# Performance work log

Hardware: AMD Instinct MI355X
Metric: run time of the kernel (lower is better)

Reference implementation:

```python
import jax, jax.numpy as jnp
import numpy as np

EPS = 1e-5
N_NODES = 50000


def sage_conv(x, src, dst, Wl, Wr, b):
    # mean-aggregate source features at destination nodes, then two linears
    msgs = x[src]  # [E, F] irregular gather
    agg = jax.ops.segment_sum(msgs, dst, num_segments=N_NODES)
    cnt = jax.ops.segment_sum(jnp.ones((src.shape[0], 1), x.dtype), dst,
                              num_segments=N_NODES)
    agg = agg / jnp.maximum(cnt, 1.0)
    return agg @ Wl + x @ Wr + b


def batch_norm(h, gamma, beta):
    mu = jnp.mean(h, axis=0)
    var = jnp.mean((h - mu) ** 2, axis=0)  # biased var, as torch BN training
    return (h - mu) * jax.lax.rsqrt(var + EPS) * gamma + beta


def setup_inputs() -> dict:
    key = jax.random.key(0)
    ks = jax.random.split(key, 16)
    d_in, d_h, n_cls, n_edges = 128, 128, 2, 600000
    s = lambda fan: 1.0 / np.sqrt(fan)
    inp = {
        "x": jax.random.normal(ks[0], (N_NODES, d_in), jnp.float32),
        "edge_index": jax.random.randint(ks[1], (2, n_edges), 0, N_NODES, jnp.int64),
        "W_l0": jax.random.uniform(ks[2], (d_in, d_h), jnp.float32, -s(d_in), s(d_in)),
        "W_r0": jax.random.uniform(ks[3], (d_in, d_h), jnp.float32, -s(d_in), s(d_in)),
        "b0": jnp.zeros((d_h,), jnp.float32),
        "g0": jnp.ones((d_h,), jnp.float32),
        "be0": jnp.zeros((d_h,), jnp.float32),
        "W_l1": jax.random.uniform(ks[4], (d_h, d_h), jnp.float32, -s(d_h), s(d_h)),
        "W_r1": jax.random.uniform(ks[5], (d_h, d_h), jnp.float32, -s(d_h), s(d_h)),
        "b1": jnp.zeros((d_h,), jnp.float32),
        "g1": jnp.ones((d_h,), jnp.float32),
        "be1": jnp.zeros((d_h,), jnp.float32),
        "W_out": jax.random.uniform(ks[6], (d_h, n_cls), jnp.float32, -s(d_h), s(d_h)),
        "b_out": jnp.zeros((n_cls,), jnp.float32),
    }
    return inp


def reference(x, edge_index, W_l0, W_r0, b0, g0, be0,
              W_l1, W_r1, b1, g1, be1, W_out, b_out):
    src, dst = edge_index[0], edge_index[1]
    # layer 0: SAGEConv -> BN -> ReLU (dropout = identity in eval/reference)
    h = sage_conv(x, src, dst, W_l0, W_r0, b0)
    h = jax.nn.relu(batch_norm(h, g0, be0))
    # layer 1
    h = sage_conv(h, src, dst, W_l1, W_r1, b1)
    h = jax.nn.relu(batch_norm(h, g1, be1))
    return h @ W_out + b_out
```

## Files before the change

kernel.cpp:

```cpp
#include <hip/hip_runtime.h>
#include <hip/hip_bf16.h>

#define F 128

typedef __attribute__((ext_vector_type(8))) short short8;
typedef __attribute__((ext_vector_type(4))) float floatx4;

__device__ __forceinline__ float bf_lo(unsigned u) { return __uint_as_float(u << 16); }
__device__ __forceinline__ float bf_hi(unsigned u) { return __uint_as_float(u & 0xffff0000u); }

__device__ __forceinline__ unsigned short f2bf(float x) {
  unsigned u = __float_as_uint(x);
  u += 0x7fffu + ((u >> 16) & 1u);
  return (unsigned short)(u >> 16);
}
__device__ __forceinline__ unsigned pack2(float a, float b) {
  return (unsigned)f2bf(a) | ((unsigned)f2bf(b) << 16);
}
__device__ __forceinline__ void add8(float* a, uint4 u) {
  a[0] += bf_lo(u.x); a[1] += bf_hi(u.x);
  a[2] += bf_lo(u.y); a[3] += bf_hi(u.y);
  a[4] += bf_lo(u.z); a[5] += bf_hi(u.z);
  a[6] += bf_lo(u.w); a[7] += bf_hi(u.w);
}

__global__ __launch_bounds__(256) void k_pre(const int* __restrict__ dst, int* __restrict__ A,
                                             int E, int cb,
                                             const float* __restrict__ x,
                                             const float* __restrict__ Wl0,
                                             const float* __restrict__ Wr0,
                                             const float* __restrict__ Wl1,
                                             const float* __restrict__ Wr1,
                                             unsigned short* __restrict__ xb,
                                             unsigned short* __restrict__ WcatT0,
                                             unsigned short* __restrict__ WcatT1, int n4) {
  if (blockIdx.x < cb) {
    int e = blockIdx.x * 256 + threadIdx.x;
    if (e < E) atomicAdd(&A[dst[e]], 1);
    return;
  }
  int i = (blockIdx.x - cb) * 256 + threadIdx.x;
  if (i < n4) {
    float4 v = ((const float4*)x)[i];
    ((ushort4*)xb)[i] = make_ushort4(f2bf(v.x), f2bf(v.y), f2bf(v.z), f2bf(v.w));
  } else {
    int j = i - n4;
    if (j < 2 * 256 * F) {
      int layer = j >> 15;
      int jj = j & 32767;
      int k = jj >> 7, n = jj & (F - 1);
      const float* Wl = layer ? Wl1 : Wl0;
      const float* Wr = layer ? Wr1 : Wr0;
      unsigned short* WT = layer ? WcatT1 : WcatT0;
      float v = (k < F) ? Wl[k * F + n] : Wr[(k - F) * F + n];
      WT[(size_t)n * 256 + k] = f2bf(v);
    }
  }
}

__global__ __launch_bounds__(1024) void k_scan(int* __restrict__ A, int* __restrict__ bsum,
                                               int* __restrict__ bases, int* __restrict__ ctl,
                                               int n, int nb) {
  __shared__ int wtot[16];
  __shared__ int lastS, sbase;
  int t = threadIdx.x, l = t & 63, w = t >> 6;
  int i = blockIdx.x * 1024 + t;
  int v = (i < n) ? A[i] : 0;
  int acc = v;
#pragma unroll
  for (int off = 1; off < 64; off <<= 1) {
    int u = __shfl_up(acc, off);
    if (l >= off) acc += u;
  }
  if (l == 63) wtot[w] = acc;
  __syncthreads();
  int woff = 0, total = 0;
#pragma unroll
  for (int ww = 0; ww < 16; ++ww) {
    total += wtot[ww];
    if (ww < w) woff += wtot[ww];
  }
  int local = woff + (acc - v);
  if (t == 0) {
    __hip_atomic_store(&bsum[blockIdx.x], total, __ATOMIC_RELEASE, __HIP_MEMORY_SCOPE_AGENT);
    int tk = __hip_atomic_fetch_add(&ctl[0], 1, __ATOMIC_ACQ_REL, __HIP_MEMORY_SCOPE_AGENT);
    lastS = (tk == nb - 1);
  }
  __syncthreads();
  if (lastS) {
    if (t < 64) {
      int bv = (t < nb) ? __hip_atomic_load(&bsum[t], __ATOMIC_ACQUIRE, __HIP_MEMORY_SCOPE_AGENT) : 0;
      int a2 = bv;
#pragma unroll
      for (int off = 1; off < 64; off <<= 1) {
        int u = __shfl_up(a2, off);
        if (t >= off) a2 += u;
      }
      if (t < nb)
        __hip_atomic_store(&bases[t], a2 - bv, __ATOMIC_RELAXED, __HIP_MEMORY_SCOPE_AGENT);
    }
    __syncthreads();
    if (t == 0) {
      __threadfence();
      __hip_atomic_store(&ctl[1], 1, __ATOMIC_RELEASE, __HIP_MEMORY_SCOPE_AGENT);
    }
  }
  if (t == 0) {
    while (__hip_atomic_load(&ctl[1], __ATOMIC_ACQUIRE, __HIP_MEMORY_SCOPE_AGENT) == 0) {}
    sbase = __hip_atomic_load(&bases[blockIdx.x], __ATOMIC_RELAXED, __HIP_MEMORY_SCOPE_AGENT);
  }
  __syncthreads();
  if (i < n) A[i] = local + sbase;
}

__global__ __launch_bounds__(256) void k_fill(const int* __restrict__ srcT,
                                              const int* __restrict__ dst,
                                              int* __restrict__ A, int* __restrict__ adj, int E) {
  int e = blockIdx.x * 256 + threadIdx.x;
  if (e >= E) return;
  int s = srcT[e], d = dst[e];
  int slot = atomicAdd(&A[d], 1);
  adj[slot] = s;
}

__global__ __launch_bounds__(256) void k_gather(const unsigned short* __restrict__ xin,
                                                const int* __restrict__ A,
                                                const int* __restrict__ adj,
                                                unsigned short* __restrict__ aggb, int N) {
  int base = blockIdx.x * 8 + ((threadIdx.x >> 6) << 1);
  int l = threadIdx.x & 63;
  int grp = l >> 4, ln = l & 15;
  const uint4* xrows = (const uint4*)xin;

  int d0 = base, d1 = base + 1;
  bool v0 = d0 < N, v1 = d1 < N;
  int e00 = 0, e01 = 0, e10 = 0, e11 = 0;
  if (v0) { e00 = (d0 == 0) ? 0 : A[d0 - 1]; e01 = A[d0]; }
  if (v1) { e10 = A[d1 - 1]; e11 = A[d1]; }
  int deg0 = e01 - e00, deg1 = e11 - e10;
  int ids0 = 0, ids1 = 0;
  if (v0 && deg0 > 0) ids0 = adj[min(e00 + l, e01 - 1)];
  if (v1 && deg1 > 0) ids1 = adj[min(e10 + l, e11 - 1)];
  int m0 = (v0 && deg0 > 0) ? min(deg0, 64) : 0;
  int m1 = (v1 && deg1 > 0) ? min(deg1, 64) : 0;
  int mm = max(m0, m1);

  float acc0[8] = {0.f, 0.f, 0.f, 0.f, 0.f, 0.f, 0.f, 0.f};
  float acc1[8] = {0.f, 0.f, 0.f, 0.f, 0.f, 0.f, 0.f, 0.f};
  for (int j0 = 0; j0 < mm; j0 += 4) {
    int jj = j0 + grp;
    int s0 = __shfl(ids0, jj);
    int s1 = __shfl(ids1, jj);
    if (jj < m0) { uint4 u = xrows[(size_t)s0 * 16 + ln]; add8(acc0, u); }
    if (jj < m1) { uint4 u = xrows[(size_t)s1 * 16 + ln]; add8(acc1, u); }
  }
  for (int e = e00 + 64 + grp; e < e01; e += 4) {
    int s = adj[e];
    uint4 u = xrows[(size_t)s * 16 + ln];
    add8(acc0, u);
  }
  for (int e = e10 + 64 + grp; e < e11; e += 4) {
    int s = adj[e];
    uint4 u = xrows[(size_t)s * 16 + ln];
    add8(acc1, u);
  }
#pragma unroll
  for (int k2 = 0; k2 < 8; ++k2) {
    acc0[k2] += __shfl_xor(acc0[k2], 16);
    acc0[k2] += __shfl_xor(acc0[k2], 32);
    acc1[k2] += __shfl_xor(acc1[k2], 16);
    acc1[k2] += __shfl_xor(acc1[k2], 32);
  }
  if (grp == 0) {
    if (v0) {
      float inv = 1.0f / fmaxf((float)deg0, 1.0f);
      uint4 o = make_uint4(pack2(acc0[0] * inv, acc0[1] * inv), pack2(acc0[2] * inv, acc0[3] * inv),
                           pack2(acc0[4] * inv, acc0[5] * inv), pack2(acc0[6] * inv, acc0[7] * inv));
      ((uint4*)aggb)[(size_t)d0 * 16 + ln] = o;
    }
    if (v1) {
      float inv = 1.0f / fmaxf((float)deg1, 1.0f);
      uint4 o = make_uint4(pack2(acc1[0] * inv, acc1[1] * inv), pack2(acc1[2] * inv, acc1[3] * inv),
                           pack2(acc1[4] * inv, acc1[5] * inv), pack2(acc1[6] * inv, acc1[7] * inv));
      ((uint4*)aggb)[(size_t)d1 * 16 + ln] = o;
    }
  }
}

__global__ __launch_bounds__(256, 2) void k_gemm(
    const unsigned short* __restrict__ aggb, const unsigned short* __restrict__ xb,
    const unsigned short* __restrict__ WcatT, const float* __restrict__ bias,
    unsigned short* __restrict__ hb, float* __restrict__ pbuf, int N) {
  const int w = threadIdx.x >> 6;
  const int l = threadIdx.x & 63;
  const int lm = l & 15;
  const int lq = l >> 4;
  const int cbase = 32 * w;

  short8 bfrag[2][8];
#pragma unroll
  for (int c = 0; c < 2; ++c) {
    int col = cbase + 16 * c + lm;
    const unsigned short* wp = WcatT + (size_t)col * 256 + lq * 8;
#pragma unroll
    for (int s = 0; s < 8; ++s) bfrag[c][s] = *(const short8*)(wp + 32 * s);
  }
  float bcol0 = bias[cbase + lm];
  float bcol1 = bias[cbase + 16 + lm];
  float bsum0 = 0.f, bsum1 = 0.f, bsq0 = 0.f, bsq1 = 0.f;

  int r0 = blockIdx.x * 64;
  floatx4 acc[4][2] = {};
#pragma unroll
  for (int t = 0; t < 4; ++t) {
    int r = r0 + 16 * t + lm;
    const unsigned short* arow = aggb + (size_t)r * F + lq * 8;
    const unsigned short* xrow = xb + (size_t)r * F + lq * 8;
    short8 af[8];
#pragma unroll
    for (int s = 0; s < 4; ++s) {
      af[s] = *(const short8*)(arow + 32 * s);
      af[s + 4] = *(const short8*)(xrow + 32 * s);
    }
#pragma unroll
    for (int s = 0; s < 8; ++s) {
      acc[t][0] = __builtin_amdgcn_mfma_f32_16x16x32_bf16(af[s], bfrag[0][s], acc[t][0], 0, 0, 0);
      acc[t][1] = __builtin_amdgcn_mfma_f32_16x16x32_bf16(af[s], bfrag[1][s], acc[t][1], 0, 0, 0);
    }
  }
#pragma unroll
  for (int t = 0; t < 4; ++t) {
#pragma unroll
    for (int c = 0; c < 2; ++c) {
      int col = cbase + 16 * c + lm;
      float bc = c ? bcol1 : bcol0;
#pragma unroll
      for (int g = 0; g < 4; ++g) {
        int row = r0 + 16 * t + lq * 4 + g;
        if (row < N) {
          float v = acc[t][c][g] + bc;
          hb[(size_t)row * F + col] = f2bf(v);
          if (c) { bsum1 += v; bsq1 += v * v; }
          else   { bsum0 += v; bsq0 += v * v; }
        }
      }
    }
  }
  bsum0 += __shfl_xor(bsum0, 16); bsum0 += __shfl_xor(bsum0, 32);
  bsq0  += __shfl_xor(bsq0, 16);  bsq0  += __shfl_xor(bsq0, 32);
  bsum1 += __shfl_xor(bsum1, 16); bsum1 += __shfl_xor(bsum1, 32);
  bsq1  += __shfl_xor(bsq1, 16);  bsq1  += __shfl_xor(bsq1, 32);
  if (lq == 0) {
    float* pb = pbuf + (size_t)blockIdx.x * 256;
    pb[cbase + lm]            = bsum0;
    pb[128 + cbase + lm]      = bsq0;
    pb[cbase + 16 + lm]       = bsum1;
    pb[128 + cbase + 16 + lm] = bsq1;
  }
}

__global__ __launch_bounds__(256) void k_bnstats(const float* __restrict__ pbuf,
                                                 const float* __restrict__ g,
                                                 const float* __restrict__ be,
                                                 float* __restrict__ stats,
                                                 float* __restrict__ scale,
                                                 float* __restrict__ shift,
                                                 float invN, int nb) {
  int t = threadIdx.x;
  float s = 0.f;
  for (int b = blockIdx.x; b < nb; b += 8) s += pbuf[(size_t)b * 256 + t];
  atomicAdd(&stats[t], s);
  __threadfence();
  __syncthreads();
  __shared__ int lastS;
  if (t == 0) {
    int ticket = atomicAdd((int*)(stats + 256), 1);
    lastS = (ticket == 7);
  }
  __syncthreads();
  if (lastS) {
    __threadfence();
    if (t < 128) {
      float sum = __hip_atomic_load(&stats[t], __ATOMIC_RELAXED, __HIP_MEMORY_SCOPE_AGENT);
      float sq  = __hip_atomic_load(&stats[t + 128], __ATOMIC_RELAXED, __HIP_MEMORY_SCOPE_AGENT);
      float mu = sum * invN;
      float var = fmaxf(sq * invN - mu * mu, 0.0f);
      float sc = g[t] * rsqrtf(var + 1e-5f);
      scale[t] = sc;
      shift[t] = be[t] - mu * sc;
    }
  }
}

__global__ __launch_bounds__(256) void k_bnrelu(const unsigned short* __restrict__ h,
                                                unsigned short* __restrict__ dst,
                                                const float* __restrict__ scale,
                                                const float* __restrict__ shift, int n8) {
  int i = blockIdx.x * 256 + threadIdx.x;
  if (i >= n8) return;
  uint4 u = ((const uint4*)h)[i];
  int g = i & 15;
  float4 sc0 = ((const float4*)scale)[2 * g];
  float4 sc1 = ((const float4*)scale)[2 * g + 1];
  float4 sh0 = ((const float4*)shift)[2 * g];
  float4 sh1 = ((const float4*)shift)[2 * g + 1];
  unsigned o0 = pack2(fmaxf(fmaf(bf_lo(u.x), sc0.x, sh0.x), 0.f),
                      fmaxf(fmaf(bf_hi(u.x), sc0.y, sh0.y), 0.f));
  unsigned o1 = pack2(fmaxf(fmaf(bf_lo(u.y), sc0.z, sh0.z), 0.f),
                      fmaxf(fmaf(bf_hi(u.y), sc0.w, sh0.w), 0.f));
  unsigned o2 = pack2(fmaxf(fmaf(bf_lo(u.z), sc1.x, sh1.x), 0.f),
                      fmaxf(fmaf(bf_hi(u.z), sc1.y, sh1.y), 0.f));
  unsigned o3 = pack2(fmaxf(fmaf(bf_lo(u.w), sc1.z, sh1.z), 0.f),
                      fmaxf(fmaf(bf_hi(u.w), sc1.w, sh1.w), 0.f));
  ((uint4*)dst)[i] = make_uint4(o0, o1, o2, o3);
}

__global__ __launch_bounds__(256) void k_bnout(const unsigned short* __restrict__ hb,
                                               const float* __restrict__ scale,
                                               const float* __restrict__ shift,
                                               const float* __restrict__ Wout,
                                               const float* __restrict__ bout,
                                               float* __restrict__ out, int N) {
  __shared__ float W0s[F], W1s[F];
  int t = threadIdx.x;
  if (t < F) {
    W0s[t] = Wout[2 * t];
    W1s[t] = Wout[2 * t + 1];
  }
  __syncthreads();
  int r = blockIdx.x * 16 + (t >> 4);
  int ln = t & 15;
  if (r >= N) return;
  uint4 u = ((const uint4*)(hb + (size_t)r * F))[ln];
  float4 sc0 = ((const float4*)scale)[2 * ln];
  float4 sc1 = ((const float4*)scale)[2 * ln + 1];
  float4 sh0 = ((const float4*)shift)[2 * ln];
  float4 sh1 = ((const float4*)shift)[2 * ln + 1];
  float v[8];
  v[0] = fmaxf(fmaf(bf_lo(u.x), sc0.x, sh0.x), 0.f);
  v[1] = fmaxf(fmaf(bf_hi(u.x), sc0.y, sh0.y), 0.f);
  v[2] = fmaxf(fmaf(bf_lo(u.y), sc0.z, sh0.z), 0.f);
  v[3] = fmaxf(fmaf(bf_hi(u.y), sc0.w, sh0.w), 0.f);
  v[4] = fmaxf(fmaf(bf_lo(u.z), sc1.x, sh1.x), 0.f);
  v[5] = fmaxf(fmaf(bf_hi(u.z), sc1.y, sh1.y), 0.f);
  v[6] = fmaxf(fmaf(bf_lo(u.w), sc1.z, sh1.z), 0.f);
  v[7] = fmaxf(fmaf(bf_hi(u.w), sc1.w, sh1.w), 0.f);
  float a0 = 0.f, a1 = 0.f;
#pragma unroll
  for (int j = 0; j < 8; ++j) {
    a0 += v[j] * W0s[8 * ln + j];
    a1 += v[j] * W1s[8 * ln + j];
  }
#pragma unroll
  for (int off = 1; off < 16; off <<= 1) {
    a0 += __shfl_xor(a0, off);
    a1 += __shfl_xor(a1, off);
  }
  if (ln == 0) {
    out[2 * r]     = a0 + bout[0];
    out[2 * r + 1] = a1 + bout[1];
  }
}

extern "C" void kernel_launch(void* const* d_in, const int* in_sizes, int n_in,
                              void* d_out, int out_size, void* d_ws, size_t ws_size,
                              hipStream_t stream) {
  const float* x   = (const float*)d_in[0];
  const int*   eix = (const int*)d_in[1];
  const float* Wl0 = (const float*)d_in[2];
  const float* Wr0 = (const float*)d_in[3];
  const float* b0  = (const float*)d_in[4];
  const float* g0  = (const float*)d_in[5];
  const float* be0 = (const float*)d_in[6];
  const float* Wl1 = (const float*)d_in[7];
  const float* Wr1 = (const float*)d_in[8];
  const float* b1  = (const float*)d_in[9];
  const float* g1  = (const float*)d_in[10];
  const float* be1 = (const float*)d_in[11];
  const float* Wo  = (const float*)d_in[12];
  const float* bo  = (const float*)d_in[13];

  int N = in_sizes[0] / F;
  int E = in_sizes[1] / 2;
  const int* src  = eix;
  const int* dstv = eix + E;

  int nRowBlocks = (N + 63) / 64;
  size_t Npad = (size_t)nRowBlocks * 64;
  int nScanB = (N + 1023) / 1024;

  unsigned short* aggb   = (unsigned short*)d_ws;
  unsigned short* xb     = aggb + Npad * F;
  unsigned short* hb     = xb + Npad * F;
  unsigned short* WcatT0 = hb + Npad * F;
  unsigned short* WcatT1 = WcatT0 + 256 * F;
  float* scale  = (float*)(WcatT1 + 256 * F);
  float* shift  = scale + F;
  int*   A      = (int*)(shift + F);
  int*   bsum   = A + N;
  int*   bases  = bsum + 64;
  int*   ctl    = bases + 64;
  float* stats0 = (float*)(ctl + 4);
  float* stats1 = stats0 + 257;
  int*   adj    = (int*)(stats1 + 257);
  float* pbuf   = (float*)(adj + E);

  hipMemsetAsync(A, 0, (size_t)(N + 132 + 514) * sizeof(int), stream);

  int n4 = N * F / 4, n8 = N * F / 8;
  int cb = (E + 255) / 256;

  k_pre<<<cb + (n4 + 2 * 256 * F + 255) / 256, 256, 0, stream>>>(
      dstv, A, E, cb, x, Wl0, Wr0, Wl1, Wr1, xb, WcatT0, WcatT1, n4);

  k_scan<<<nScanB, 1024, 0, stream>>>(A, bsum, bases, ctl, N, nScanB);
  k_fill<<<(E + 255) / 256, 256, 0, stream>>>(src, dstv, A, adj, E);

  k_gather<<<(N + 7) / 8, 256, 0, stream>>>(xb, A, adj, aggb, N);
  k_gemm<<<nRowBlocks, 256, 0, stream>>>(aggb, xb, WcatT0, b0, hb, pbuf, N);
  k_bnstats<<<8, 256, 0, stream>>>(pbuf, g0, be0, stats0, scale, shift, 1.0f / N, nRowBlocks);
  k_bnrelu<<<(n8 + 255) / 256, 256, 0, stream>>>(hb, xb, scale, shift, n8);

  k_gather<<<(N + 7) / 8, 256, 0, stream>>>(xb, A, adj, aggb, N);
  k_gemm<<<nRowBlocks, 256, 0, stream>>>(aggb, xb, WcatT1, b1, hb, pbuf, N);
  k_bnstats<<<8, 256, 0, stream>>>(pbuf, g1, be1, stats1, scale, shift, 1.0f / N, nRowBlocks);

  k_bnout<<<(N + 15) / 16, 256, 0, stream>>>(hb, scale, shift, Wo, bo, (float*)d_out, N);
}
```

Measured before the change: 339.7 us.

## Fuse scan with CSR fill and simplify gather to 16 lanes per node

The prefix-scan kernel now also performs the CSR adjacency fill after a device-wide atomic barrier, removing one kernel launch. The fill loop is grid-strided over the few scan blocks. The gather kernel is rewritten so each 16-lane group handles one destination node with a 4-way unrolled neighbor loop, replacing the two-nodes-per-wave shuffle scheme. The risks are lower parallelism in the fill phase (only nScanB blocks) and a grid barrier that assumes all blocks are co-resident.

```diff
diff --git a/kernel.cpp b/kernel.cpp
--- a/kernel.cpp
+++ b/kernel.cpp
@@ -58,9 +58,12 @@
   }
 }
 
-__global__ __launch_bounds__(1024) void k_scan(int* __restrict__ A, int* __restrict__ bsum,
-                                               int* __restrict__ bases, int* __restrict__ ctl,
-                                               int n, int nb) {
+__global__ __launch_bounds__(1024) void k_scanfill(int* __restrict__ A, int* __restrict__ bsum,
+                                                   int* __restrict__ bases, int* __restrict__ ctl,
+                                                   int n, int nb,
+                                                   const int* __restrict__ srcT,
+                                                   const int* __restrict__ dstv,
+                                                   int* __restrict__ adj, int E) {
   __shared__ int wtot[16];
   __shared__ int lastS, sbase;
   int t = threadIdx.x, l = t & 63, w = t >> 6;
@@ -110,81 +113,54 @@
     sbase = __hip_atomic_load(&bases[blockIdx.x], __ATOMIC_RELAXED, __HIP_MEMORY_SCOPE_AGENT);
   }
   __syncthreads();
-  if (i < n) A[i] = local + sbase;
-}
-
-__global__ __launch_bounds__(256) void k_fill(const int* __restrict__ srcT,
-                                              const int* __restrict__ dst,
-                                              int* __restrict__ A, int* __restrict__ adj, int E) {
-  int e = blockIdx.x * 256 + threadIdx.x;
-  if (e >= E) return;
-  int s = srcT[e], d = dst[e];
-  int slot = atomicAdd(&A[d], 1);
-  adj[slot] = s;
+  if (i < n)
+    __hip_atomic_store(&A[i], local + sbase, __ATOMIC_RELAXED, __HIP_MEMORY_SCOPE_AGENT);
+  __syncthreads();
+  if (t == 0) {
+    __hip_atomic_fetch_add(&ctl[2], 1, __ATOMIC_ACQ_REL, __HIP_MEMORY_SCOPE_AGENT);
+    while (__hip_atomic_load(&ctl[2], __ATOMIC_ACQUIRE, __HIP_MEMORY_SCOPE_AGENT) < nb) {}
+  }
+  __syncthreads();
+  int nthr = nb * 1024;
+  for (int e = blockIdx.x * 1024 + t; e < E; e += nthr) {
+    int s = srcT[e], d = dstv[e];
+    int slot = atomicAdd(&A[d], 1);
+    adj[slot] = s;
+  }
 }
 
 __global__ __launch_bounds__(256) void k_gather(const unsigned short* __restrict__ xin,
                                                 const int* __restrict__ A,
                                                 const int* __restrict__ adj,
                                                 unsigned short* __restrict__ aggb, int N) {
-  int base = blockIdx.x * 8 + ((threadIdx.x >> 6) << 1);
-  int l = threadIdx.x & 63;
-  int grp = l >> 4, ln = l & 15;
+  int d = blockIdx.x * 16 + (threadIdx.x >> 4);
+  int ln = threadIdx.x & 15;
+  if (d >= N) return;
   const uint4* xrows = (const uint4*)xin;
-
-  int d0 = base, d1 = base + 1;
-  bool v0 = d0 < N, v1 = d1 < N;
-  int e00 = 0, e01 = 0, e10 = 0, e11 = 0;
-  if (v0) { e00 = (d0 == 0) ? 0 : A[d0 - 1]; e01 = A[d0]; }
-  if (v1) { e10 = A[d1 - 1]; e11 = A[d1]; }
-  int deg0 = e01 - e00, deg1 = e11 - e10;
-  int ids0 = 0, ids1 = 0;
-  if (v0 && deg0 > 0) ids0 = adj[min(e00 + l, e01 - 1)];
-  if (v1 && deg1 > 0) ids1 = adj[min(e10 + l, e11 - 1)];
-  int m0 = (v0 && deg0 > 0) ? min(deg0, 64) : 0;
-  int m1 = (v1 && deg1 > 0) ? min(deg1, 64) : 0;
-  int mm = max(m0, m1);
-
-  float acc0[8] = {0.f, 0.f, 0.f, 0.f, 0.f, 0.f, 0.f, 0.f};
-  float acc1[8] = {0.f, 0.f, 0.f, 0.f, 0.f, 0.f, 0.f, 0.f};
-  for (int j0 = 0; j0 < mm; j0 += 4) {
-    int jj = j0 + grp;
-    int s0 = __shfl(ids0, jj);
-    int s1 = __shfl(ids1, jj);
-    if (jj < m0) { uint4 u = xrows[(size_t)s0 * 16 + ln]; add8(acc0, u); }
-    if (jj < m1) { uint4 u = xrows[(size_t)s1 * 16 + ln]; add8(acc1, u); }
-  }
-  for (int e = e00 + 64 + grp; e < e01; e += 4) {
-    int s = adj[e];
-    uint4 u = xrows[(size_t)s * 16 + ln];
-    add8(acc0, u);
-  }
-  for (int e = e10 + 64 + grp; e < e11; e += 4) {
-    int s = adj[e];
-    uint4 u = xrows[(size_t)s * 16 + ln];
-    add8(acc1, u);
-  }
-#pragma unroll
-  for (int k2 = 0; k2 < 8; ++k2) {
-    acc0[k2] += __shfl_xor(acc0[k2], 16);
-    acc0[k2] += __shfl_xor(acc0[k2], 32);
-    acc1[k2] += __shfl_xor(acc1[k2], 16);
-    acc1[k2] += __shfl_xor(acc1[k2], 32);
-  }
-  if (grp == 0) {
-    if (v0) {
-      float inv = 1.0f / fmaxf((float)deg0, 1.0f);
-      uint4 o = make_uint4(pack2(acc0[0] * inv, acc0[1] * inv), pack2(acc0[2] * inv, acc0[3] * inv),
-                           pack2(acc0[4] * inv, acc0[5] * inv), pack2(acc0[6] * inv, acc0[7] * inv));
-      ((uint4*)aggb)[(size_t)d0 * 16 + ln] = o;
-    }
-    if (v1) {
-      float inv = 1.0f / fmaxf((float)deg1, 1.0f);
-      uint4 o = make_uint4(pack2(acc1[0] * inv, acc1[1] * inv), pack2(acc1[2] * inv, acc1[3] * inv),
-                           pack2(acc1[4] * inv, acc1[5] * inv), pack2(acc1[6] * inv, acc1[7] * inv));
-      ((uint4*)aggb)[(size_t)d1 * 16 + ln] = o;
-    }
-  }
+  int e0 = (d == 0) ? 0 : A[d - 1];
+  int e1 = A[d];
+  int deg = e1 - e0;
+  float acc[8] = {0.f, 0.f, 0.f, 0.f, 0.f, 0.f, 0.f, 0.f};
+  int e = e0;
+  for (; e + 4 <= e1; e += 4) {
+    int s0 = adj[e], s1 = adj[e + 1], s2 = adj[e + 2], s3 = adj[e + 3];
+    uint4 u0 = xrows[(size_t)s0 * 16 + ln];
+    uint4 u1 = xrows[(size_t)s1 * 16 + ln];
+    uint4 u2 = xrows[(size_t)s2 * 16 + ln];
+    uint4 u3 = xrows[(size_t)s3 * 16 + ln];
+    add8(acc, u0);
+    add8(acc, u1);
+    add8(acc, u2);
+    add8(acc, u3);
+  }
+  for (; e < e1; ++e) {
+    uint4 u = xrows[(size_t)adj[e] * 16 + ln];
+    add8(acc, u);
+  }
+  float inv = 1.0f / fmaxf((float)deg, 1.0f);
+  uint4 o = make_uint4(pack2(acc[0] * inv, acc[1] * inv), pack2(acc[2] * inv, acc[3] * inv),
+                       pack2(acc[4] * inv, acc[5] * inv), pack2(acc[6] * inv, acc[7] * inv));
+  ((uint4*)aggb)[(size_t)d * 16 + ln] = o;
 }
 
 __global__ __launch_bounds__(256, 2) void k_gemm(
@@ -413,15 +389,14 @@
   k_pre<<<cb + (n4 + 2 * 256 * F + 255) / 256, 256, 0, stream>>>(
       dstv, A, E, cb, x, Wl0, Wr0, Wl1, Wr1, xb, WcatT0, WcatT1, n4);
 
-  k_scan<<<nScanB, 1024, 0, stream>>>(A, bsum, bases, ctl, N, nScanB);
-  k_fill<<<(E + 255) / 256, 256, 0, stream>>>(src, dstv, A, adj, E);
-
-  k_gather<<<(N + 7) / 8, 256, 0, stream>>>(xb, A, adj, aggb, N);
+  k_scanfill<<<nScanB, 1024, 0, stream>>>(A, bsum, bases, ctl, N, nScanB, src, dstv, adj, E);
+
+  k_gather<<<(N + 15) / 16, 256, 0, stream>>>(xb, A, adj, aggb, N);
   k_gemm<<<nRowBlocks, 256, 0, stream>>>(aggb, xb, WcatT0, b0, hb, pbuf, N);
   k_bnstats<<<8, 256, 0, stream>>>(pbuf, g0, be0, stats0, scale, shift, 1.0f / N, nRowBlocks);
   k_bnrelu<<<(n8 + 255) / 256, 256, 0, stream>>>(hb, xb, scale, shift, n8);
 
-  k_gather<<<(N + 7) / 8, 256, 0, stream>>>(xb, A, adj, aggb, N);
+  k_gather<<<(N + 15) / 16, 256, 0, stream>>>(xb, A, adj, aggb, N);
   k_gemm<<<nRowBlocks, 256, 0, stream>>>(aggb, xb, WcatT1, b1, hb, pbuf, N);
   k_bnstats<<<8, 256, 0, stream>>>(pbuf, g1, be1, stats1, scale, shift, 1.0f / N, nRowBlocks);
 
```

After: 348.0 us. 2.4% more time.
